# Kernel tuning notes

Hardware: AMD Instinct MI355X
Metric: run time of the kernel (lower is better)

Reference implementation:

```python
import jax, jax.numpy as jnp
import numpy as np

B, S, D, H, W = 4, 9, 256, 32, 32
RATIO = 2
NH = 16
DK = D // NH            # 16 (module recomputes d_k = d_in // n_head)
HP, WP = H // RATIO, W // RATIO
QL = H * W              # 1024 query tokens
KL = S * HP * WP        # 2304 key/value tokens


def setup_inputs() -> dict:
    key = jax.random.key(0)
    ks = jax.random.split(key, 8)
    s = 0.02
    return {
        "x": jax.random.normal(ks[0], (B, S, D, H, W), jnp.float32),
        "conv_w": jax.random.normal(ks[1], (D, D, RATIO, RATIO), jnp.float32) * s,
        "conv_b": jnp.zeros((D,), jnp.float32),
        "gn_g": jnp.ones((D,), jnp.float32),
        "gn_b": jnp.zeros((D,), jnp.float32),
        "wq": jax.random.normal(ks[2], (D, NH * DK), jnp.float32) * s,
        "bq": jnp.zeros((NH * DK,), jnp.float32),
        "wkv": jax.random.normal(ks[3], (D, 2 * NH * DK), jnp.float32) * s,
        "bkv": jnp.zeros((2 * NH * DK,), jnp.float32),
        "pos_bias": jax.random.normal(ks[4], (NH, QL, KL), jnp.float32) * s,
        "proj_w": jax.random.normal(ks[5], (D, D), jnp.float32) * s,
        "proj_b": jnp.zeros((D,), jnp.float32),
    }


def reference(x, conv_w, conv_b, gn_g, gn_b, wq, bq, wkv, bkv, pos_bias, proj_w, proj_b):
    b, s, d, h, w = x.shape
    hp, wp = h // RATIO, w // RATIO

    # query stream: center frame, flattened -> (b, h*w, d)
    v_self = x[:, 4].reshape(b, d, h * w).transpose(0, 2, 1)

    # key/value stream: Conv2d(k=stride=ratio) + GroupNorm(NH groups) over all frames
    vn = x.reshape(b * s, d, h, w)
    vn = jax.lax.conv_general_dilated(
        vn, conv_w, window_strides=(RATIO, RATIO), padding="VALID",
        dimension_numbers=("NCHW", "OIHW", "NCHW"))
    vn = vn + conv_b[None, :, None, None]
    g = vn.reshape(b * s, NH, d // NH, hp, wp)
    mu = g.mean(axis=(2, 3, 4), keepdims=True)
    var = g.var(axis=(2, 3, 4), keepdims=True)
    g = (g - mu) * jax.lax.rsqrt(var + 1e-5)
    vn = g.reshape(b * s, d, hp, wp) * gn_g[None, :, None, None] + gn_b[None, :, None, None]
    # (b, s*hp*wp, d)
    vn = vn.reshape(b, s, d, hp, wp).transpose(0, 1, 3, 4, 2).reshape(b, s * hp * wp, d)

    # projections
    q = (v_self @ wq + bq).reshape(b, h * w, NH, DK)            # (b, Q, H, dk)
    kv = (vn @ wkv + bkv).reshape(b, -1, 2, NH, DK)             # (b, K, 2, H, dk)
    k, v = kv[:, :, 0], kv[:, :, 1]                             # (b, K, H, dk)

    # cross-attention with learned positional bias added to QK^T
    dots = jnp.einsum("bqhd,bkhd->hbqk", q, k) * (DK ** -0.5)
    dots = dots + pos_bias[:, None]                             # (H, b, Q, K)
    attn = jax.nn.softmax(dots, axis=-1)
    out = jnp.einsum("hbqk,bkhd->bqhd", attn, v)                # (b, Q, H, dk)
    out = out.reshape(b, h, w, NH * DK)                         # (n c) head-major
    out = out @ proj_w + proj_b                                 # (b, h, w, d)

    # SpatialVit: 'b h w c -> b c h w'
    return out.transpose(0, 3, 1, 2)
```

## Files before the change

kernel.cpp:

```cpp
#include <hip/hip_runtime.h>

#define NBATCH 4
#define NSEQ   9
#define ND     256
#define NHEAD  16
#define NDKv   16
#define NQ     1024
#define NKL    2304
#define NSAMP  36

constexpr long OFF_CONV = 0;
constexpr long OFF_VN   = 2359296;
constexpr long OFF_WT   = 3538944;
constexpr long OFF_Q    = 4718592;
constexpr long OFF_K    = 5242880;
constexpr long OFF_VT   = 6422528;
constexpr long OFF_AO   = 0;

using bf16x8 = __attribute__((ext_vector_type(8))) short;
using f32x4  = __attribute__((ext_vector_type(4))) float;

__device__ __forceinline__ float bf2f(unsigned short h) {
    unsigned int u = ((unsigned int)h) << 16;
    float f; __builtin_memcpy(&f, &u, 4); return f;
}
__device__ __forceinline__ unsigned short f2bf(float f) {
    unsigned int u; __builtin_memcpy(&u, &f, 4);
    u += 0x7fffu + ((u >> 16) & 1u);
    return (unsigned short)(u >> 16);
}
template<bool BF> __device__ __forceinline__ float ld1(const void* p, long i) {
    if constexpr (BF) return bf2f(((const unsigned short*)p)[i]);
    else return ((const float*)p)[i];
}
template<bool BF> __device__ __forceinline__ float2 ld2(const void* p, long i) {
    if constexpr (BF) { ushort2 v = *(const ushort2*)((const unsigned short*)p + i);
                        return make_float2(bf2f(v.x), bf2f(v.y)); }
    else return *(const float2*)((const float*)p + i);
}
template<bool BF> __device__ __forceinline__ float4 ld4(const void* p, long i) {
    if constexpr (BF) { ushort4 v = *(const ushort4*)((const unsigned short*)p + i);
                        return make_float4(bf2f(v.x), bf2f(v.y), bf2f(v.z), bf2f(v.w)); }
    else return *(const float4*)((const float*)p + i);
}
template<bool BF> __device__ __forceinline__ void st1(void* p, long i, float v) {
    if constexpr (BF) ((unsigned short*)p)[i] = f2bf(v);
    else ((float*)p)[i] = v;
}
__device__ __forceinline__ bool detect_bf16(const void* gn_g) {
    return (*(const unsigned int*)gn_g) != 0x3F800000u;
}

template<bool BF>
__device__ void conv_body(const void* __restrict__ x, const void* __restrict__ cw,
                          const void* __restrict__ cb, float* __restrict__ ws) {
    __shared__ short lA[64 * 40];
    __shared__ short lB[128 * 40];
    const int tid  = threadIdx.x;
    const int n    = blockIdx.x;
    const int pq   = blockIdx.y;
    const int och  = blockIdx.z;
    const int wave = tid >> 6, lane = tid & 63;
    const int col  = lane & 15, quad = lane >> 4;

    f32x4 acc[4][2];
    #pragma unroll
    for (int mt = 0; mt < 4; ++mt)
        #pragma unroll
        for (int nt = 0; nt < 2; ++nt) acc[mt][nt] = {0.f, 0.f, 0.f, 0.f};

    const int icl  = tid >> 5;
    const int t5   = tid & 31;
    const int ihl  = t5 >> 2;
    const int iwg  = (t5 & 3) * 8;
    const int k0x  = icl * 4 + (ihl & 1) * 2;
    const int posx = (ihl >> 1) * 16 + (iwg >> 1);
    const long xrow = ((long)n * ND * 32 + (long)(pq * 8 + ihl)) * 32 + iwg;

    const int ocw = tid >> 3;
    const int kkw = (tid & 7) * 4;

    for (int kc = 0; kc < 32; ++kc) {
        __syncthreads();
        {
            const long xa = xrow + (long)(kc * 8 + icl) * 1024;
            float4 v0 = ld4<BF>(x, xa);
            float4 v1 = ld4<BF>(x, xa + 4);
            unsigned short us[8] = {f2bf(v0.x), f2bf(v0.y), f2bf(v0.z), f2bf(v0.w),
                                    f2bf(v1.x), f2bf(v1.y), f2bf(v1.z), f2bf(v1.w)};
            #pragma unroll
            for (int o = 0; o < 4; ++o)
                *(ushort2*)&lA[(posx + o) * 40 + k0x] = make_ushort2(us[2*o], us[2*o+1]);
        }
        #pragma unroll
        for (int j = 0; j < 4; ++j) {
            const int oc = ocw + j * 32;
            float4 wv = ld4<BF>(cw, (long)(och * 128 + oc) * 1024 + kc * 32 + kkw);
            unsigned int lo = (unsigned int)f2bf(wv.x) | ((unsigned int)f2bf(wv.y) << 16);
            unsigned int hi = (unsigned int)f2bf(wv.z) | ((unsigned int)f2bf(wv.w) << 16);
            *(uint2*)&lB[oc * 40 + kkw] = make_uint2(lo, hi);
        }
        __syncthreads();
        bf16x8 af[4];
        #pragma unroll
        for (int mt = 0; mt < 4; ++mt)
            af[mt] = *(const bf16x8*)&lA[(mt * 16 + col) * 40 + quad * 8];
        #pragma unroll
        for (int nt = 0; nt < 2; ++nt) {
            bf16x8 bfg = *(const bf16x8*)&lB[((wave * 2 + nt) * 16 + col) * 40 + quad * 8];
            #pragma unroll
            for (int mt = 0; mt < 4; ++mt)
                acc[mt][nt] = __builtin_amdgcn_mfma_f32_16x16x32_bf16(af[mt], bfg, acc[mt][nt], 0, 0, 0);
        }
    }

    float* co = ws + OFF_CONV + (long)n * 65536;
    #pragma unroll
    for (int nt = 0; nt < 2; ++nt) {
        const int oc = och * 128 + (wave * 2 + nt) * 16 + col;
        const float cbv = ld1<BF>(cb, oc);
        #pragma unroll
        for (int mt = 0; mt < 4; ++mt)
            #pragma unroll
            for (int r = 0; r < 4; ++r) {
                const int pos = pq * 64 + mt * 16 + quad * 4 + r;
                co[(long)pos * 256 + oc] = acc[mt][nt][r] + cbv;
            }
    }
}
__global__ void __launch_bounds__(256)
conv_k(const void* x, const void* cw, const void* cb, const void* gg, float* ws) {
    if (detect_bf16(gg)) conv_body<true>(x, cw, cb, ws);
    else                 conv_body<false>(x, cw, cb, ws);
}

template<bool BF>
__device__ void gn_body(const void* __restrict__ gn_g, const void* __restrict__ gn_b,
                        float* __restrict__ ws) {
    const int t = threadIdx.x;
    const int n = blockIdx.x;
    const int g = blockIdx.y;
    const float* row = ws + OFF_CONV + ((long)n * 256 + t) * 256 + g * 16;

    float v[16]; float s1 = 0.f, s2 = 0.f;
    #pragma unroll
    for (int q4 = 0; q4 < 4; ++q4) {
        float4 a = *(const float4*)(row + q4 * 4);
        v[q4*4+0] = a.x; v[q4*4+1] = a.y; v[q4*4+2] = a.z; v[q4*4+3] = a.w;
        s1 += (a.x + a.y) + (a.z + a.w);
        s2 += (a.x*a.x + a.y*a.y) + (a.z*a.z + a.w*a.w);
    }
    __shared__ float r1[4], r2[4];
    #pragma unroll
    for (int off = 32; off > 0; off >>= 1) {
        s1 += __shfl_down(s1, off, 64);
        s2 += __shfl_down(s2, off, 64);
    }
    if ((t & 63) == 0) { r1[t >> 6] = s1; r2[t >> 6] = s2; }
    __syncthreads();
    const float ts1 = r1[0] + r1[1] + r1[2] + r1[3];
    const float ts2 = r2[0] + r2[1] + r2[2] + r2[3];
    const float mean = ts1 * (1.0f / 4096.0f);
    const float var  = ts2 * (1.0f / 4096.0f) - mean * mean;
    const float inv  = rsqrtf(var + 1e-5f);

    const int b = n / NSEQ, s = n % NSEQ;
    float o[16];
    #pragma unroll
    for (int cl = 0; cl < 16; ++cl) {
        float gg = ld1<BF>(gn_g, g * 16 + cl);
        float bb = ld1<BF>(gn_b, g * 16 + cl);
        o[cl] = (v[cl] - mean) * inv * gg + bb;
    }
    unsigned short* dst = (unsigned short*)(ws + OFF_VN)
                          + ((long)b * NKL + s * 256 + t) * ND + g * 16;
    bf16x8 w0, w1;
    #pragma unroll
    for (int cl = 0; cl < 8; ++cl) {
        w0[cl] = (short)f2bf(o[cl]);
        w1[cl] = (short)f2bf(o[cl + 8]);
    }
    *(bf16x8*)dst       = w0;
    *(bf16x8*)(dst + 8) = w1;
}
__global__ void gn_k(const void* gg, const void* gb, float* ws) {
    if (detect_bf16(gg)) gn_body<true>(gg, gb, ws);
    else                 gn_body<false>(gg, gb, ws);
}

template<bool BF>
__device__ void tw_body(const void* __restrict__ wkv, float* __restrict__ ws) {
    __shared__ float tile[16][17];
    const int t = threadIdx.x;
    const int oc0 = blockIdx.x * 16;
    const int r = t >> 4, c = t & 15;
    unsigned short* wt = (unsigned short*)(ws + OFF_WT);
    for (int k0 = 0; k0 < ND; k0 += 16) {
        const float v = ld1<BF>(wkv, (long)(k0 + r) * 512 + oc0 + c);
        __syncthreads();
        tile[r][c] = v;
        __syncthreads();
        wt[(long)(oc0 + r) * ND + k0 + c] = f2bf(tile[c][r]);
    }
}
__global__ void __launch_bounds__(256)
tw_k(const void* wkv, const void* gg, float* ws) {
    if (detect_bf16(gg)) tw_body<true>(wkv, ws);
    else                 tw_body<false>(wkv, ws);
}

template<bool BF>
__device__ void q_body(const void* __restrict__ x, const void* __restrict__ wq,
                       const void* __restrict__ bq, float* __restrict__ ws) {
    const int lane = threadIdx.x;
    const int mb = blockIdx.x;
    const int ob = blockIdx.y;
    const int b  = mb >> 6;
    const int q0 = (mb & 63) * 16;
    const int oc = ob * 64 + lane;

    float acc[16];
    const float bqv = ld1<BF>(bq, oc);
    #pragma unroll
    for (int i = 0; i < 16; ++i) acc[i] = bqv;

    const long xoff = ((long)(b * NSEQ + 4) * ND) * NQ;
    for (int d = 0; d < ND; ++d) {
        const float wv = ld1<BF>(wq, (long)d * 256 + oc);
        const long vb = xoff + (long)d * NQ + q0;
        float4 a0 = ld4<BF>(x, vb + 0);
        float4 a1 = ld4<BF>(x, vb + 4);
        float4 a2 = ld4<BF>(x, vb + 8);
        float4 a3 = ld4<BF>(x, vb + 12);
        acc[0]  += a0.x * wv; acc[1]  += a0.y * wv; acc[2]  += a0.z * wv; acc[3]  += a0.w * wv;
        acc[4]  += a1.x * wv; acc[5]  += a1.y * wv; acc[6]  += a1.z * wv; acc[7]  += a1.w * wv;
        acc[8]  += a2.x * wv; acc[9]  += a2.y * wv; acc[10] += a2.z * wv; acc[11] += a2.w * wv;
        acc[12] += a3.x * wv; acc[13] += a3.y * wv; acc[14] += a3.z * wv; acc[15] += a3.w * wv;
    }
    const int h = oc >> 4, dk = oc & 15;
    unsigned short* qb = (unsigned short*)(ws + OFF_Q);
    #pragma unroll
    for (int i = 0; i < 16; ++i)
        qb[(((long)b * NHEAD + h) * NQ + q0 + i) * NDKv + dk] = f2bf(acc[i]);
}
__global__ void __launch_bounds__(64, 4)
q_k(const void* x, const void* wq, const void* bq, const void* gg, float* ws) {
    if (detect_bf16(gg)) q_body<true>(x, wq, bq, ws);
    else                 q_body<false>(x, wq, bq, ws);
}

template<bool BF>
__device__ void kv_body(const void* __restrict__ bkv, float* __restrict__ ws) {
    __shared__ short lA[64 * 32];
    __shared__ short lB[128 * 32];
    const int tid = threadIdx.x;
    const int b   = blockIdx.x / 36;
    const int t0  = (blockIdx.x % 36) * 64;
    const int ob  = blockIdx.y;
    const int wave = tid >> 6, lane = tid & 63;
    const int col = lane & 15, quad = lane >> 4;

    const unsigned short* vnb = (const unsigned short*)(ws + OFF_VN) + ((long)b * NKL + t0) * ND;
    const unsigned short* wtb = (const unsigned short*)(ws + OFF_WT) + (long)ob * 128 * ND;

    const int rS = tid >> 2;
    const int sS = (tid & 3) * 8;

    f32x4 acc[4][2];
    #pragma unroll
    for (int mt = 0; mt < 4; ++mt)
        #pragma unroll
        for (int nt = 0; nt < 2; ++nt) acc[mt][nt] = {0.f, 0.f, 0.f, 0.f};

    for (int kc = 0; kc < 8; ++kc) {
        __syncthreads();
        *(bf16x8*)&lA[rS * 32 + sS] =
            *(const bf16x8*)(vnb + (long)rS * ND + kc * 32 + sS);
        *(bf16x8*)&lB[rS * 32 + sS] =
            *(const bf16x8*)(wtb + (long)rS * ND + kc * 32 + sS);
        *(bf16x8*)&lB[(64 + rS) * 32 + sS] =
            *(const bf16x8*)(wtb + (long)(64 + rS) * ND + kc * 32 + sS);
        __syncthreads();
        bf16x8 af[4];
        #pragma unroll
        for (int mt = 0; mt < 4; ++mt)
            af[mt] = *(const bf16x8*)&lA[(mt * 16 + col) * 32 + quad * 8];
        #pragma unroll
        for (int nt = 0; nt < 2; ++nt) {
            bf16x8 bfg = *(const bf16x8*)&lB[((wave * 2 + nt) * 16 + col) * 32 + quad * 8];
            #pragma unroll
            for (int mt = 0; mt < 4; ++mt)
                acc[mt][nt] = __builtin_amdgcn_mfma_f32_16x16x32_bf16(af[mt], bfg, acc[mt][nt], 0, 0, 0);
        }
    }

    const bool isv = (ob >= 2);
    unsigned short* k16  = (unsigned short*)(ws + OFF_K);
    unsigned short* vt16 = (unsigned short*)(ws + OFF_VT);
    #pragma unroll
    for (int nt = 0; nt < 2; ++nt) {
        const int ocl = (wave * 2 + nt) * 16 + col;
        const int oc  = ob * 128 + ocl;
        const float bv = ld1<BF>(bkv, oc);
        const int oc2 = oc & 255, h = oc2 >> 4, dk = oc2 & 15;
        if (!isv) {
            #pragma unroll
            for (int mt = 0; mt < 4; ++mt)
                #pragma unroll
                for (int r = 0; r < 4; ++r) {
                    const int tok = t0 + mt * 16 + quad * 4 + r;
                    k16[((long)(b * NHEAD + h) * NKL + tok) * NDKv + dk] = f2bf(acc[mt][nt][r] + bv);
                }
        } else {
            #pragma unroll
            for (int mt = 0; mt < 4; ++mt) {
                const int tok = t0 + mt * 16 + quad * 4;
                ushort4 pk;
                pk.x = f2bf(acc[mt][nt][0] + bv);
                pk.y = f2bf(acc[mt][nt][1] + bv);
                pk.z = f2bf(acc[mt][nt][2] + bv);
                pk.w = f2bf(acc[mt][nt][3] + bv);
                *(ushort4*)&vt16[((long)(b * NHEAD + h) * 16 + dk) * NKL + tok] = pk;
            }
        }
    }
}
__global__ void __launch_bounds__(256)
kv_k(const void* bkv, const void* gg, float* ws) {
    if (detect_bf16(gg)) kv_body<true>(bkv, ws);
    else                 kv_body<false>(bkv, ws);
}

template<bool BF>
__device__ void attn_body(const void* __restrict__ pos_bias, float* __restrict__ ws) {
    __shared__ short lds[4 * 16 * 40];
    const int tid  = threadIdx.x;
    const int b    = tid >> 6;
    const int lane = tid & 63;
    const int qt = blockIdx.x;
    const int h  = blockIdx.y;
    const int bh = b * NHEAD + h;
    const int col  = lane & 15;
    const int quad = lane >> 4;
    short* myl = &lds[b * 640];

    const unsigned short* Qb = (const unsigned short*)(ws + OFF_Q);
    const unsigned short* Kb = (const unsigned short*)(ws + OFF_K);
    const unsigned short* Vt = (const unsigned short*)(ws + OFF_VT);

    bf16x8 qfrag = {0,0,0,0,0,0,0,0};
    if (quad < 2)
        qfrag = *(const bf16x8*)(Qb + (((long)bh * NQ + qt * 16 + col) * 16 + quad * 8));

    const unsigned short* Krows = Kb + (long)bh * NKL * 16 + (long)col * 16 + (quad & 1) * 8;
    const unsigned short* Vrow  = Vt + ((long)bh * 16 + col) * NKL + quad * 8;
    const long pbase = ((long)h * NQ + qt * 16 + col) * NKL + quad * 4;

    f32x4 oacc = {0.f, 0.f, 0.f, 0.f};
    const f32x4 zc = {0.f, 0.f, 0.f, 0.f};
    float lsum = 0.f;

    bf16x8 kf0 = *(const bf16x8*)(Krows);
    bf16x8 kf1 = *(const bf16x8*)(Krows + 16L * 16);
    bf16x8 vf  = *(const bf16x8*)(Vrow);
    float4 pb0 = ld4<BF>(pos_bias, pbase);
    float4 pb1 = ld4<BF>(pos_bias, pbase + 16);

    for (int kb = 0; kb < NKL; kb += 32) {
        const bf16x8 ck0 = kf0, ck1 = kf1, cv = vf;
        const float4 cb0 = pb0, cb1 = pb1;
        const int nkb = (kb + 32 < NKL) ? kb + 32 : 0;
        kf0 = *(const bf16x8*)(Krows + (long)nkb * 16);
        kf1 = *(const bf16x8*)(Krows + (long)(nkb + 16) * 16);
        vf  = *(const bf16x8*)(Vrow + nkb);
        pb0 = ld4<BF>(pos_bias, pbase + nkb);
        pb1 = ld4<BF>(pos_bias, pbase + nkb + 16);

        f32x4 s0 = __builtin_amdgcn_mfma_f32_16x16x32_bf16(ck0, qfrag, zc, 0, 0, 0);
        f32x4 s1 = __builtin_amdgcn_mfma_f32_16x16x32_bf16(ck1, qfrag, zc, 0, 0, 0);

        float p0 = __expf(s0[0] * 0.25f + cb0.x);
        float p1 = __expf(s0[1] * 0.25f + cb0.y);
        float p2 = __expf(s0[2] * 0.25f + cb0.z);
        float p3 = __expf(s0[3] * 0.25f + cb0.w);
        float r0 = __expf(s1[0] * 0.25f + cb1.x);
        float r1 = __expf(s1[1] * 0.25f + cb1.y);
        float r2 = __expf(s1[2] * 0.25f + cb1.z);
        float r3 = __expf(s1[3] * 0.25f + cb1.w);
        lsum += ((p0 + p1) + (p2 + p3)) + ((r0 + r1) + (r2 + r3));

        unsigned int lo0 = (unsigned int)f2bf(p0) | ((unsigned int)f2bf(p1) << 16);
        unsigned int hi0 = (unsigned int)f2bf(p2) | ((unsigned int)f2bf(p3) << 16);
        unsigned int lo1 = (unsigned int)f2bf(r0) | ((unsigned int)f2bf(r1) << 16);
        unsigned int hi1 = (unsigned int)f2bf(r2) | ((unsigned int)f2bf(r3) << 16);
        *(uint2*)(&myl[col * 40 + quad * 4])      = make_uint2(lo0, hi0);
        *(uint2*)(&myl[col * 40 + 16 + quad * 4]) = make_uint2(lo1, hi1);

        bf16x8 pfrag = *(const bf16x8*)(&myl[col * 40 + quad * 8]);
        oacc = __builtin_amdgcn_mfma_f32_16x16x32_bf16(pfrag, cv, oacc, 0, 0, 0);
    }

    lsum += __shfl_xor(lsum, 16, 64);
    lsum += __shfl_xor(lsum, 32, 64);

    float* ao = ws + OFF_AO + (((long)b * NQ + qt * 16) * ND) + h * 16 + col;
    #pragma unroll
    for (int r = 0; r < 4; ++r) {
        float Lr = __shfl(lsum, quad * 4 + r, 64);
        ao[(long)(quad * 4 + r) * ND] = oacc[r] * (1.0f / Lr);
    }
}
__global__ void __launch_bounds__(256)
attn_k(const void* pos_bias, const void* gg, float* ws) {
    if (detect_bf16(gg)) attn_body<true>(pos_bias, ws);
    else                 attn_body<false>(pos_bias, ws);
}

template<bool BF>
__device__ void proj_body(const void* __restrict__ pw, const void* __restrict__ pbias,
                          const float* __restrict__ ws, void* __restrict__ out) {
    const int lane = threadIdx.x;
    const int bp = blockIdx.x;
    const int cbk = blockIdx.y;
    const int b = bp >> 4;
    const int p = (bp & 15) * 64 + lane;
    const int c0 = cbk * 16;

    const float* ao = ws + OFF_AO + ((long)b * NQ + p) * ND;
    float acc[16];
    #pragma unroll
    for (int i = 0; i < 16; ++i) acc[i] = ld1<BF>(pbias, c0 + i);

    for (int j = 0; j < ND; j += 4) {
        const float4 av = *(const float4*)(ao + j);
        #pragma unroll
        for (int jj = 0; jj < 4; ++jj) {
            const float a = (jj == 0) ? av.x : (jj == 1) ? av.y : (jj == 2) ? av.z : av.w;
            #pragma unroll
            for (int i = 0; i < 16; ++i) {
                const float w = ld1<BF>(pw, (long)(j + jj) * ND + c0 + i);
                acc[i] += a * w;
            }
        }
    }
    #pragma unroll
    for (int i = 0; i < 16; ++i)
        st1<BF>(out, ((long)b * ND + c0 + i) * NQ + p, acc[i]);
}
__global__ void __launch_bounds__(64, 4)
proj_k(const void* pw, const void* pbias, const void* gg, const float* ws, void* out) {
    if (detect_bf16(gg)) proj_body<true>(pw, pbias, ws, out);
    else                 proj_body<false>(pw, pbias, ws, out);
}

extern "C" void kernel_launch(void* const* d_in, const int* in_sizes, int n_in,
                              void* d_out, int out_size, void* d_ws, size_t ws_size,
                              hipStream_t stream) {
    (void)in_sizes; (void)n_in; (void)out_size; (void)ws_size;
    const void* x   = d_in[0];
    const void* cw  = d_in[1];
    const void* cb  = d_in[2];
    const void* gg  = d_in[3];
    const void* gb  = d_in[4];
    const void* wq  = d_in[5];
    const void* bq  = d_in[6];
    const void* wkv = d_in[7];
    const void* bkv = d_in[8];
    const void* pb  = d_in[9];
    const void* pw  = d_in[10];
    const void* pbb = d_in[11];
    float* ws = (float*)d_ws;

    conv_k   <<<dim3(36, 4, 2), 256, 0, stream>>>(x, cw, cb, gg, ws);
    gn_k     <<<dim3(36, 16),   256, 0, stream>>>(gg, gb, ws);
    tw_k     <<<dim3(32),       256, 0, stream>>>(wkv, gg, ws);
    q_k      <<<dim3(256, 4),    64, 0, stream>>>(x, wq, bq, gg, ws);
    kv_k     <<<dim3(144, 4),   256, 0, stream>>>(bkv, gg, ws);
    attn_k   <<<dim3(64, 16),   256, 0, stream>>>(pb, gg, ws);
    proj_k   <<<dim3(64, 16),    64, 0, stream>>>(pw, pbb, gg, ws, d_out);
}
```

Before: 511.7 us.

## Split attention key range across two blocks and combine partials in new kernel

Attention work is split along the key dimension into two halves (grid z=2). Each half writes unnormalized partial outputs and row sums to workspace, and a new combine kernel adds them and normalizes. The pos_bias prefetch is also made deeper by unrolling two chunks per iteration, and launch bounds now request higher occupancy. This doubles block count to improve GPU fill at the cost of an extra kernel launch and partial-sum traffic.

Result: no change. 517.1 us (+1.1%).

```diff
diff --git a/kernel.cpp b/kernel.cpp
--- a/kernel.cpp
+++ b/kernel.cpp
@@ -7,6 +7,7 @@
 #define NDKv   16
 #define NQ     1024
 #define NKL    2304
+#define NKLH   1152
 #define NSAMP  36
 
 constexpr long OFF_CONV = 0;
@@ -16,6 +17,8 @@
 constexpr long OFF_K    = 5242880;
 constexpr long OFF_VT   = 6422528;
 constexpr long OFF_AO   = 0;
+constexpr long OFF_PN   = 1048576;
+constexpr long OFF_PL   = 3145728;
 
 using bf16x8 = __attribute__((ext_vector_type(8))) short;
 using f32x4  = __attribute__((ext_vector_type(4))) float;
@@ -32,11 +35,6 @@
 template<bool BF> __device__ __forceinline__ float ld1(const void* p, long i) {
     if constexpr (BF) return bf2f(((const unsigned short*)p)[i]);
     else return ((const float*)p)[i];
-}
-template<bool BF> __device__ __forceinline__ float2 ld2(const void* p, long i) {
-    if constexpr (BF) { ushort2 v = *(const ushort2*)((const unsigned short*)p + i);
-                        return make_float2(bf2f(v.x), bf2f(v.y)); }
-    else return *(const float2*)((const float*)p + i);
 }
 template<bool BF> __device__ __forceinline__ float4 ld4(const void* p, long i) {
     if constexpr (BF) { ushort4 v = *(const ushort4*)((const unsigned short*)p + i);
@@ -337,8 +335,10 @@
     const int tid  = threadIdx.x;
     const int b    = tid >> 6;
     const int lane = tid & 63;
-    const int qt = blockIdx.x;
-    const int h  = blockIdx.y;
+    const int qt   = blockIdx.x;
+    const int h    = blockIdx.y;
+    const int half = blockIdx.z;
+    const int t0   = half * NKLH;
     const int bh = b * NHEAD + h;
     const int col  = lane & 15;
     const int quad = lane >> 4;
@@ -352,33 +352,17 @@
     if (quad < 2)
         qfrag = *(const bf16x8*)(Qb + (((long)bh * NQ + qt * 16 + col) * 16 + quad * 8));
 
-    const unsigned short* Krows = Kb + (long)bh * NKL * 16 + (long)col * 16 + (quad & 1) * 8;
-    const unsigned short* Vrow  = Vt + ((long)bh * 16 + col) * NKL + quad * 8;
-    const long pbase = ((long)h * NQ + qt * 16 + col) * NKL + quad * 4;
+    const unsigned short* Krows = Kb + ((long)bh * NKL + t0) * 16 + (long)col * 16 + (quad & 1) * 8;
+    const unsigned short* Vrow  = Vt + ((long)bh * 16 + col) * NKL + t0 + quad * 8;
+    const long pbase = ((long)h * NQ + qt * 16 + col) * NKL + t0 + quad * 4;
 
     f32x4 oacc = {0.f, 0.f, 0.f, 0.f};
     const f32x4 zc = {0.f, 0.f, 0.f, 0.f};
     float lsum = 0.f;
 
-    bf16x8 kf0 = *(const bf16x8*)(Krows);
-    bf16x8 kf1 = *(const bf16x8*)(Krows + 16L * 16);
-    bf16x8 vf  = *(const bf16x8*)(Vrow);
-    float4 pb0 = ld4<BF>(pos_bias, pbase);
-    float4 pb1 = ld4<BF>(pos_bias, pbase + 16);
-
-    for (int kb = 0; kb < NKL; kb += 32) {
-        const bf16x8 ck0 = kf0, ck1 = kf1, cv = vf;
-        const float4 cb0 = pb0, cb1 = pb1;
-        const int nkb = (kb + 32 < NKL) ? kb + 32 : 0;
-        kf0 = *(const bf16x8*)(Krows + (long)nkb * 16);
-        kf1 = *(const bf16x8*)(Krows + (long)(nkb + 16) * 16);
-        vf  = *(const bf16x8*)(Vrow + nkb);
-        pb0 = ld4<BF>(pos_bias, pbase + nkb);
-        pb1 = ld4<BF>(pos_bias, pbase + nkb + 16);
-
+    auto do_chunk = [&](bf16x8 ck0, bf16x8 ck1, bf16x8 cv, float4 cb0, float4 cb1) {
         f32x4 s0 = __builtin_amdgcn_mfma_f32_16x16x32_bf16(ck0, qfrag, zc, 0, 0, 0);
         f32x4 s1 = __builtin_amdgcn_mfma_f32_16x16x32_bf16(ck1, qfrag, zc, 0, 0, 0);
-
         float p0 = __expf(s0[0] * 0.25f + cb0.x);
         float p1 = __expf(s0[1] * 0.25f + cb0.y);
         float p2 = __expf(s0[2] * 0.25f + cb0.z);
@@ -388,32 +372,84 @@
         float r2 = __expf(s1[2] * 0.25f + cb1.z);
         float r3 = __expf(s1[3] * 0.25f + cb1.w);
         lsum += ((p0 + p1) + (p2 + p3)) + ((r0 + r1) + (r2 + r3));
-
         unsigned int lo0 = (unsigned int)f2bf(p0) | ((unsigned int)f2bf(p1) << 16);
         unsigned int hi0 = (unsigned int)f2bf(p2) | ((unsigned int)f2bf(p3) << 16);
         unsigned int lo1 = (unsigned int)f2bf(r0) | ((unsigned int)f2bf(r1) << 16);
         unsigned int hi1 = (unsigned int)f2bf(r2) | ((unsigned int)f2bf(r3) << 16);
         *(uint2*)(&myl[col * 40 + quad * 4])      = make_uint2(lo0, hi0);
         *(uint2*)(&myl[col * 40 + 16 + quad * 4]) = make_uint2(lo1, hi1);
-
         bf16x8 pfrag = *(const bf16x8*)(&myl[col * 40 + quad * 8]);
         oacc = __builtin_amdgcn_mfma_f32_16x16x32_bf16(pfrag, cv, oacc, 0, 0, 0);
+    };
+
+    bf16x8 kf0 = *(const bf16x8*)(Krows);
+    bf16x8 kf1 = *(const bf16x8*)(Krows + 16L * 16);
+    bf16x8 vf  = *(const bf16x8*)(Vrow);
+    float4 pbA0 = ld4<BF>(pos_bias, pbase);
+    float4 pbA1 = ld4<BF>(pos_bias, pbase + 16);
+    float4 pbB0 = ld4<BF>(pos_bias, pbase + 32);
+    float4 pbB1 = ld4<BF>(pos_bias, pbase + 48);
+
+    for (int kb = 0; kb < NKLH; kb += 64) {
+        {
+            const bf16x8 ck0 = kf0, ck1 = kf1, cv = vf;
+            const float4 cb0 = pbA0, cb1 = pbA1;
+            const int nk = kb + 32;
+            kf0 = *(const bf16x8*)(Krows + (long)nk * 16);
+            kf1 = *(const bf16x8*)(Krows + (long)(nk + 16) * 16);
+            vf  = *(const bf16x8*)(Vrow + nk);
+            const int pk = (kb + 64 < NKLH) ? kb + 64 : 0;
+            pbA0 = ld4<BF>(pos_bias, pbase + pk);
+            pbA1 = ld4<BF>(pos_bias, pbase + pk + 16);
+            do_chunk(ck0, ck1, cv, cb0, cb1);
+        }
+        {
+            const bf16x8 ck0 = kf0, ck1 = kf1, cv = vf;
+            const float4 cb0 = pbB0, cb1 = pbB1;
+            const int nk = (kb + 64 < NKLH) ? kb + 64 : 0;
+            kf0 = *(const bf16x8*)(Krows + (long)nk * 16);
+            kf1 = *(const bf16x8*)(Krows + (long)(nk + 16) * 16);
+            vf  = *(const bf16x8*)(Vrow + nk);
+            const int pk = (kb + 96 < NKLH) ? kb + 96 : 0;
+            pbB0 = ld4<BF>(pos_bias, pbase + pk);
+            pbB1 = ld4<BF>(pos_bias, pbase + pk + 16);
+            do_chunk(ck0, ck1, cv, cb0, cb1);
+        }
     }
 
     lsum += __shfl_xor(lsum, 16, 64);
     lsum += __shfl_xor(lsum, 32, 64);
 
-    float* ao = ws + OFF_AO + (((long)b * NQ + qt * 16) * ND) + h * 16 + col;
-    #pragma unroll
-    for (int r = 0; r < 4; ++r) {
-        float Lr = __shfl(lsum, quad * 4 + r, 64);
-        ao[(long)(quad * 4 + r) * ND] = oacc[r] * (1.0f / Lr);
-    }
-}
-__global__ void __launch_bounds__(256)
+    float* pn = ws + OFF_PN + ((((long)half * NBATCH + b) * NHEAD + h) * NQ + qt * 16) * 16;
+    #pragma unroll
+    for (int r = 0; r < 4; ++r)
+        pn[(long)(quad * 4 + r) * 16 + col] = oacc[r];
+    if (quad == 0) {
+        float* pl = ws + OFF_PL + (((long)half * NBATCH + b) * NHEAD + h) * NQ + qt * 16;
+        pl[col] = lsum;
+    }
+}
+__global__ void __launch_bounds__(256, 8)
 attn_k(const void* pos_bias, const void* gg, float* ws) {
     if (detect_bf16(gg)) attn_body<true>(pos_bias, ws);
     else                 attn_body<false>(pos_bias, ws);
+}
+
+__global__ void __launch_bounds__(256)
+comb_k(float* __restrict__ ws) {
+    const int idx = blockIdx.x * 256 + threadIdx.x;
+    const int b   = idx >> 18;
+    const int rem = idx & 262143;
+    const int q   = rem >> 8;
+    const int c   = rem & 255;
+    const int h   = c >> 4, dv = c & 15;
+    const float* pn = ws + OFF_PN;
+    const float* pl = ws + OFF_PL;
+    const long base0 = (((long)b * NHEAD + h) * NQ + q);
+    const long base1 = ((((long)NBATCH + b) * NHEAD + h) * NQ + q);
+    const float n = pn[base0 * 16 + dv] + pn[base1 * 16 + dv];
+    const float l = pl[base0] + pl[base1];
+    ws[OFF_AO + idx] = n / l;
 }
 
 template<bool BF>
@@ -476,6 +512,7 @@
     tw_k     <<<dim3(32),       256, 0, stream>>>(wkv, gg, ws);
     q_k      <<<dim3(256, 4),    64, 0, stream>>>(x, wq, bq, gg, ws);
     kv_k     <<<dim3(144, 4),   256, 0, stream>>>(bkv, gg, ws);
-    attn_k   <<<dim3(64, 16),   256, 0, stream>>>(pb, gg, ws);
+    attn_k   <<<dim3(64, 16, 2), 256, 0, stream>>>(pb, gg, ws);
+    comb_k   <<<dim3(4096),     256, 0, stream>>>(ws);
     proj_k   <<<dim3(64, 16),    64, 0, stream>>>(pw, pbb, gg, ws, d_out);
 }
```
